# Kernel tuning notes

Measured on AMD Instinct MI355X. Metric: run time of the kernel, lower is better.

## Reference

```python
import jax, jax.numpy as jnp
import numpy as np

H, D = 16, 64  # num_heads, head_dim (d_model = 1024)


def setup_inputs() -> dict:
    key = jax.random.key(0)
    ks = jax.random.split(key, 5)
    B, S, E = 2, 2048, H * D
    scale = 0.02  # keep logits in a sane range
    return {
        "x": jax.random.normal(ks[0], (B, S, E), jnp.float32),
        "Wq": jax.random.normal(ks[1], (E, E), jnp.float32) * scale,
        "bq": jnp.zeros((E,), jnp.float32),
        "Wk": jax.random.normal(ks[2], (E, E), jnp.float32) * scale,
        "bk": jnp.zeros((E,), jnp.float32),
        "Wv": jax.random.normal(ks[3], (E, E), jnp.float32) * scale,
        "bv": jnp.zeros((E,), jnp.float32),
        "Wo": jax.random.normal(ks[4], (E, E), jnp.float32) * scale,
        "bo": jnp.zeros((E,), jnp.float32),
    }


def reference(x, Wq, bq, Wk, bk, Wv, bv, Wo, bo):
    B, S, E = x.shape

    def proj(W, b):
        # torch nn.Linear: x @ W.T + b; then split heads -> [B, H, S, D]
        return (x @ W.T + b).reshape(B, S, H, D).transpose(0, 2, 1, 3)

    q = proj(Wq, bq)
    k = proj(Wk, bk)
    v = proj(Wv, bv)

    # scores [B, H, S, S]; original masks with -inf BEFORE scaling (-inf/scale == -inf)
    att = jnp.einsum("bhqd,bhkd->bhqk", q, k)
    causal = jnp.triu(jnp.ones((S, S), bool), k=1)  # True above diagonal
    att = jnp.where(causal, -jnp.inf, att) * jnp.float32(1.0 / np.sqrt(D))
    att = jax.nn.softmax(att, axis=-1)

    ctx = jnp.einsum("bhqk,bhkd->bhqd", att, v)  # [B, H, S, D]
    ctx = ctx.transpose(0, 2, 1, 3).reshape(B, S, H * D)  # merge heads
    return ctx @ Wo.T + bo
```

## Files before the change

kernel.cpp:

```cpp
#include <hip/hip_runtime.h>
#include <hip/hip_bf16.h>

#define S_LEN 2048
#define NH    16
#define HD    64
#define EMB   1024
#define BATCH 2
#define M_TOT 4096

typedef __attribute__((ext_vector_type(8)))  __bf16   bf16x8;
typedef __attribute__((ext_vector_type(4)))  __bf16   bf16x4;
typedef __attribute__((ext_vector_type(4)))  float    f32x4;
typedef __attribute__((ext_vector_type(16))) float    f32x16;
typedef __attribute__((ext_vector_type(4)))  unsigned u32x4;

static __device__ __forceinline__ unsigned pk2(float a, float b) {
    unsigned short ua = __builtin_bit_cast(unsigned short, (__bf16)a);
    unsigned short ub = __builtin_bit_cast(unsigned short, (__bf16)b);
    return (unsigned)ua | ((unsigned)ub << 16);
}

__global__ __launch_bounds__(256) void cast_all(const float* __restrict__ x,
        const float* __restrict__ wq, const float* __restrict__ wk,
        const float* __restrict__ wv, const float* __restrict__ wo,
        __bf16* __restrict__ xb, __bf16* __restrict__ wqb,
        __bf16* __restrict__ wkb, __bf16* __restrict__ wvb,
        __bf16* __restrict__ wob) {
    int i = blockIdx.x * 256 + threadIdx.x;
    const float* src; __bf16* dst; int j;
    if (i < (1 << 20)) { src = x; dst = xb; j = i; }
    else {
        int t = i - (1 << 20);
        int r = t >> 18;
        j = t & ((1 << 18) - 1);
        src = (r == 0) ? wq : (r == 1) ? wk : (r == 2) ? wv : wo;
        dst = (r == 0) ? wqb : (r == 1) ? wkb : (r == 2) ? wvb : wob;
    }
    f32x4 v = ((const f32x4*)src)[j];
    bf16x4 o;
    o[0] = (__bf16)v[0]; o[1] = (__bf16)v[1];
    o[2] = (__bf16)v[2]; o[3] = (__bf16)v[3];
    ((bf16x4*)dst)[j] = o;
}

#define GEMM_STAGE(Abuf, Bbuf, Asrc, Bsrc, k0)                                            \
    _Pragma("unroll")                                                                     \
    for (int t = 0; t < 4; ++t) {                                                         \
        const int row = wid * 32 + t * 8;                                                 \
        __builtin_amdgcn_global_load_lds(                                                 \
            (const __attribute__((address_space(1))) void*)&Asrc[(size_t)(m0 + row + lr8) * EMB + (k0) + lc8], \
            (__attribute__((address_space(3))) void*)&Abuf[row][0], 16, 0, 0);            \
        __builtin_amdgcn_global_load_lds(                                                 \
            (const __attribute__((address_space(1))) void*)&Bsrc[(size_t)(n0 + row + lr8) * EMB + (k0) + lc8], \
            (__attribute__((address_space(3))) void*)&Bbuf[row][0], 16, 0, 0);            \
    }

#define GEMM_COMPUTE(Abuf, Bbuf)                                                          \
    _Pragma("unroll")                                                                     \
    for (int kk = 0; kk < 2; ++kk) {                                                      \
        bf16x8 af[4], bfr[4];                                                             \
        _Pragma("unroll")                                                                 \
        for (int i = 0; i < 4; ++i)                                                       \
            af[i] = *(const bf16x8*)&Abuf[wr * 64 + i * 16 + lrow][kk * 32 + lhi * 8];    \
        _Pragma("unroll")                                                                 \
        for (int j = 0; j < 4; ++j)                                                       \
            bfr[j] = *(const bf16x8*)&Bbuf[wc * 64 + j * 16 + lrow][kk * 32 + lhi * 8];   \
        _Pragma("unroll")                                                                 \
        for (int i = 0; i < 4; ++i)                                                       \
            _Pragma("unroll")                                                             \
            for (int j = 0; j < 4; ++j)                                                   \
                acc[i][j] = __builtin_amdgcn_mfma_f32_16x16x32_bf16(af[i], bfr[j], acc[i][j], 0, 0, 0); \
    }

__global__ __launch_bounds__(256) void gemm_qkv(const __bf16* __restrict__ A,
        const __bf16* __restrict__ Wq, const __bf16* __restrict__ Wk,
        const __bf16* __restrict__ Wv,
        const float* __restrict__ bq, const float* __restrict__ bk,
        const float* __restrict__ bv,
        __bf16* __restrict__ Qo, __bf16* __restrict__ Ko, __bf16* __restrict__ Vo) {
    __shared__ __bf16 As0[128][64], As1[128][64];
    __shared__ __bf16 Bs0[128][64], Bs1[128][64];

    const int z = blockIdx.z;
    const __bf16* Bw   = (z == 0) ? Wq : (z == 1) ? Wk : Wv;
    const float*  bias = (z == 0) ? bq : (z == 1) ? bk : bv;
    __bf16*       outp = (z == 0) ? Qo : (z == 1) ? Ko : Vo;

    const int tid  = threadIdx.x;
    const int wid  = tid >> 6;
    const int lane = tid & 63;
    const int lrow = lane & 15;
    const int lhi  = lane >> 4;
    const int m0 = blockIdx.y * 128;
    const int n0 = blockIdx.x * 128;
    const int wr = wid >> 1, wc = wid & 1;
    const int lr8 = lane >> 3;
    const int lc8 = (lane & 7) * 8;

    f32x4 acc[4][4];
#pragma unroll
    for (int i = 0; i < 4; ++i)
#pragma unroll
        for (int j = 0; j < 4; ++j)
            acc[i][j] = (f32x4){0.f, 0.f, 0.f, 0.f};

    GEMM_STAGE(As0, Bs0, A, Bw, 0)
    __syncthreads();
    for (int kt = 0; kt < 16; kt += 2) {
        GEMM_STAGE(As1, Bs1, A, Bw, (kt + 1) * 64)
        GEMM_COMPUTE(As0, Bs0)
        __syncthreads();
        if (kt + 2 < 16) { GEMM_STAGE(As0, Bs0, A, Bw, (kt + 2) * 64) }
        GEMM_COMPUTE(As1, Bs1)
        __syncthreads();
    }

#pragma unroll
    for (int i = 0; i < 4; ++i) {
#pragma unroll
        for (int j = 0; j < 4; ++j) {
#pragma unroll
            for (int jj = 0; jj < 4; ++jj) {
                int row = m0 + wr * 64 + i * 16 + lhi * 4 + jj;
                int col = n0 + wc * 64 + j * 16 + lrow;
                float v = acc[i][j][jj] + bias[col];
                int b = row >> 11, s = row & (S_LEN - 1);
                int h = col >> 6,  d = col & (HD - 1);
                size_t idx = (z == 2)
                    ? ((size_t)(b * NH + h) * HD + d) * S_LEN + s
                    : ((size_t)(b * NH + h) * S_LEN + s) * HD + d;
                outp[idx] = (__bf16)v;
            }
        }
    }
}

__global__ __launch_bounds__(256) void gemm_out(const __bf16* __restrict__ A,
        const __bf16* __restrict__ Bw, const float* __restrict__ bias,
        float* __restrict__ outp) {
    __shared__ __bf16 As0[128][64], As1[128][64];
    __shared__ __bf16 Bs0[128][64], Bs1[128][64];

    const int tid  = threadIdx.x;
    const int wid  = tid >> 6;
    const int lane = tid & 63;
    const int lrow = lane & 15;
    const int lhi  = lane >> 4;
    const int m0 = blockIdx.y * 128;
    const int n0 = blockIdx.x * 128;
    const int wr = wid >> 1, wc = wid & 1;
    const int lr8 = lane >> 3;
    const int lc8 = (lane & 7) * 8;

    f32x4 acc[4][4];
#pragma unroll
    for (int i = 0; i < 4; ++i)
#pragma unroll
        for (int j = 0; j < 4; ++j)
            acc[i][j] = (f32x4){0.f, 0.f, 0.f, 0.f};

    GEMM_STAGE(As0, Bs0, A, Bw, 0)
    __syncthreads();
    for (int kt = 0; kt < 16; kt += 2) {
        GEMM_STAGE(As1, Bs1, A, Bw, (kt + 1) * 64)
        GEMM_COMPUTE(As0, Bs0)
        __syncthreads();
        if (kt + 2 < 16) { GEMM_STAGE(As0, Bs0, A, Bw, (kt + 2) * 64) }
        GEMM_COMPUTE(As1, Bs1)
        __syncthreads();
    }

#pragma unroll
    for (int i = 0; i < 4; ++i)
#pragma unroll
        for (int j = 0; j < 4; ++j)
#pragma unroll
            for (int jj = 0; jj < 4; ++jj) {
                int row = m0 + wr * 64 + i * 16 + lhi * 4 + jj;
                int col = n0 + wc * 64 + j * 16 + lrow;
                outp[(size_t)row * EMB + col] = acc[i][j][jj] + bias[col];
            }
}

__global__ __launch_bounds__(256) void attn_kernel(const __bf16* __restrict__ Q,
        const __bf16* __restrict__ K, const __bf16* __restrict__ Vt,
        __bf16* __restrict__ ctx) {
    __shared__ float Of[4][32][65];
    __shared__ float MLs[4][2][32];

    const int wid  = threadIdx.x >> 6;
    const int lane = threadIdx.x & 63;
    const int lq   = lane & 31;
    const int hi   = lane >> 5;
    const int bid  = blockIdx.x;
    const int xcd  = bid & 7;
    const int idx  = bid >> 3;
    const int qt   = 63 - (idx & 63);
    const int bh   = xcd + 8 * (idx >> 6);
    const int q0   = qt * 32;

    const __bf16* Qh = Q  + (size_t)bh * S_LEN * HD;
    const __bf16* Kh = K  + (size_t)bh * S_LEN * HD;
    const __bf16* Vh = Vt + (size_t)bh * HD * S_LEN;

    bf16x8 qf[4];
#pragma unroll
    for (int ds = 0; ds < 4; ++ds) {
        bf16x8 t = *(const bf16x8*)&Qh[(size_t)(q0 + lq) * HD + ds * 16 + hi * 8];
#pragma unroll
        for (int j = 0; j < 8; ++j) qf[ds][j] = (__bf16)((float)t[j] * 0.125f);
    }

    f32x16 o0, o1;
#pragma unroll
    for (int r = 0; r < 16; ++r) { o0[r] = 0.f; o1[r] = 0.f; }
    float m = -1e30f, l = 0.f;

    const int nkt = qt + 1;

    bf16x8 kf0, kf1, kf2, kf3;
    if (wid < nkt) {
        const __bf16* kp = &Kh[(size_t)(wid * 32 + lq) * HD + hi * 8];
        kf0 = *(const bf16x8*)(kp);      kf1 = *(const bf16x8*)(kp + 16);
        kf2 = *(const bf16x8*)(kp + 32); kf3 = *(const bf16x8*)(kp + 48);
    }

    for (int kt = wid; kt < nkt; kt += 4) {
        const int kk0 = kt * 32;

        bf16x8 va0 = *(const bf16x8*)&Vh[(size_t)lq * S_LEN + kk0 + hi * 8];
        bf16x8 vb0 = *(const bf16x8*)&Vh[(size_t)lq * S_LEN + kk0 + 16 + hi * 8];
        bf16x8 va1 = *(const bf16x8*)&Vh[(size_t)(32 + lq) * S_LEN + kk0 + hi * 8];
        bf16x8 vb1 = *(const bf16x8*)&Vh[(size_t)(32 + lq) * S_LEN + kk0 + 16 + hi * 8];

        const int nk0 = (kt + 4 < nkt ? kt + 4 : kt) * 32;
        bf16x8 nkf0, nkf1, nkf2, nkf3;
        {
            const __bf16* kp = &Kh[(size_t)(nk0 + lq) * HD + hi * 8];
            nkf0 = *(const bf16x8*)(kp);      nkf1 = *(const bf16x8*)(kp + 16);
            nkf2 = *(const bf16x8*)(kp + 32); nkf3 = *(const bf16x8*)(kp + 48);
        }

        f32x16 s;
#pragma unroll
        for (int r = 0; r < 16; ++r) s[r] = 0.f;
        s = __builtin_amdgcn_mfma_f32_32x32x16_bf16(kf0, qf[0], s, 0, 0, 0);
        s = __builtin_amdgcn_mfma_f32_32x32x16_bf16(kf1, qf[1], s, 0, 0, 0);
        s = __builtin_amdgcn_mfma_f32_32x32x16_bf16(kf2, qf[2], s, 0, 0, 0);
        s = __builtin_amdgcn_mfma_f32_32x32x16_bf16(kf3, qf[3], s, 0, 0, 0);

        if (kk0 == q0) {
#pragma unroll
            for (int r = 0; r < 16; ++r) {
                int keyl = (r & 3) + 8 * (r >> 2) + 4 * hi;
                s[r] = (keyl <= lq) ? s[r] : -1e30f;
            }
        }

        float pm = s[0];
#pragma unroll
        for (int r = 1; r < 16; ++r) pm = fmaxf(pm, s[r]);
        pm = fmaxf(pm, __shfl_xor(pm, 32));

        if (!__all(pm - m <= 8.f)) {
            float mn = fmaxf(m, pm);
            float f  = __expf(m - mn);
            l *= f;
#pragma unroll
            for (int r = 0; r < 16; ++r) { o0[r] *= f; o1[r] *= f; }
            m = mn;
        }

        float ps = 0.f;
#pragma unroll
        for (int r = 0; r < 16; ++r) { s[r] = __expf(s[r] - m); ps += s[r]; }
        ps += __shfl_xor(ps, 32);
        l += ps;

        unsigned w0 = pk2(s[0],  s[1]),  w1 = pk2(s[2],  s[3]);
        unsigned w2 = pk2(s[4],  s[5]),  w3 = pk2(s[6],  s[7]);
        unsigned w4 = pk2(s[8],  s[9]),  w5 = pk2(s[10], s[11]);
        unsigned w6 = pk2(s[12], s[13]), w7 = pk2(s[14], s[15]);

        unsigned e0 = (unsigned)__shfl_xor((int)(hi ? w0 : w2), 32);
        unsigned e1 = (unsigned)__shfl_xor((int)(hi ? w1 : w3), 32);
        unsigned e2 = (unsigned)__shfl_xor((int)(hi ? w4 : w6), 32);
        unsigned e3 = (unsigned)__shfl_xor((int)(hi ? w5 : w7), 32);
        u32x4 pb0, pb1;
        pb0[0] = hi ? e0 : w0;  pb0[1] = hi ? e1 : w1;
        pb0[2] = hi ? w2 : e0;  pb0[3] = hi ? w3 : e1;
        pb1[0] = hi ? e2 : w4;  pb1[1] = hi ? e3 : w5;
        pb1[2] = hi ? w6 : e2;  pb1[3] = hi ? w7 : e3;
        bf16x8 pb0b = __builtin_bit_cast(bf16x8, pb0);
        bf16x8 pb1b = __builtin_bit_cast(bf16x8, pb1);

        o0 = __builtin_amdgcn_mfma_f32_32x32x16_bf16(va0, pb0b, o0, 0, 0, 0);
        o0 = __builtin_amdgcn_mfma_f32_32x32x16_bf16(vb0, pb1b, o0, 0, 0, 0);
        o1 = __builtin_amdgcn_mfma_f32_32x32x16_bf16(va1, pb0b, o1, 0, 0, 0);
        o1 = __builtin_amdgcn_mfma_f32_32x32x16_bf16(vb1, pb1b, o1, 0, 0, 0);

        kf0 = nkf0; kf1 = nkf1; kf2 = nkf2; kf3 = nkf3;
    }

#pragma unroll
    for (int r = 0; r < 16; ++r) {
        int d0 = (r & 3) + 8 * (r >> 2) + 4 * hi;
        Of[wid][lq][d0]      = o0[r];
        Of[wid][lq][32 + d0] = o1[r];
    }
    if (lane < 32) { MLs[wid][0][lq] = m; MLs[wid][1][lq] = l; }
    __syncthreads();

    {
        const int tq = threadIdx.x >> 3;
        const int d8 = (threadIdx.x & 7) * 8;
        float m0_ = MLs[0][0][tq], m1_ = MLs[1][0][tq];
        float m2_ = MLs[2][0][tq], m3_ = MLs[3][0][tq];
        float M = fmaxf(fmaxf(m0_, m1_), fmaxf(m2_, m3_));
        float a0 = __expf(m0_ - M), a1 = __expf(m1_ - M);
        float a2 = __expf(m2_ - M), a3 = __expf(m3_ - M);
        float L = MLs[0][1][tq] * a0 + MLs[1][1][tq] * a1
                + MLs[2][1][tq] * a2 + MLs[3][1][tq] * a3;
        float invL = 1.f / L;
        const int b = bh >> 4, h = bh & 15;
        bf16x8 outv;
#pragma unroll
        for (int e = 0; e < 8; ++e) {
            int d = d8 + e;
            float v = a0 * Of[0][tq][d] + a1 * Of[1][tq][d]
                    + a2 * Of[2][tq][d] + a3 * Of[3][tq][d];
            outv[e] = (__bf16)(v * invL);
        }
        *(bf16x8*)&ctx[((size_t)b * S_LEN + q0 + tq) * EMB + h * HD + d8] = outv;
    }
}

extern "C" void kernel_launch(void* const* d_in, const int* in_sizes, int n_in,
                              void* d_out, int out_size, void* d_ws, size_t ws_size,
                              hipStream_t stream) {
    const float* x  = (const float*)d_in[0];
    const float* Wq = (const float*)d_in[1];
    const float* bq = (const float*)d_in[2];
    const float* Wk = (const float*)d_in[3];
    const float* bk = (const float*)d_in[4];
    const float* Wv = (const float*)d_in[5];
    const float* bv = (const float*)d_in[6];
    const float* Wo = (const float*)d_in[7];
    const float* bo = (const float*)d_in[8];

    char* ws = (char*)d_ws;
    __bf16* xb  = (__bf16*)(ws);
    __bf16* Wqb = (__bf16*)(ws + ( 8ull << 20));
    __bf16* Wkb = (__bf16*)(ws + (10ull << 20));
    __bf16* Wvb = (__bf16*)(ws + (12ull << 20));
    __bf16* Wob = (__bf16*)(ws + (14ull << 20));
    __bf16* Qb  = (__bf16*)(ws + (16ull << 20));
    __bf16* Kb  = (__bf16*)(ws + (24ull << 20));
    __bf16* Vtb = (__bf16*)(ws + (32ull << 20));
    __bf16* Cb  = (__bf16*)(ws + (40ull << 20));

    cast_all<<<8192, 256, 0, stream>>>(x, Wq, Wk, Wv, Wo, xb, Wqb, Wkb, Wvb, Wob);

    gemm_qkv<<<dim3(EMB / 128, M_TOT / 128, 3), 256, 0, stream>>>(
        xb, Wqb, Wkb, Wvb, bq, bk, bv, Qb, Kb, Vtb);

    attn_kernel<<<dim3(2048), 256, 0, stream>>>(Qb, Kb, Vtb, Cb);

    gemm_out<<<dim3(EMB / 128, M_TOT / 128), 256, 0, stream>>>(Cb, Wob, bo, (float*)d_out);
}
```

Measured before the change: 238.8 us.

## Fuse Q/K/V projections into one GEMM kernel sharing the A tile

Replaces the three-way z-dimension launch of the QKV GEMM with a single 512-thread block that loads one activation tile and three weight tiles, computing Q, K and V accumulators together. This cuts redundant loads of the activation matrix across the three projections. In exchange it drops the previous LDS double-buffering, so global-to-LDS loads are no longer overlapped with MFMA compute. The grid also shrinks to a third as many blocks, and each block holds more accumulator registers.

Result: faster. 232.6 us (-2.6%).

```diff
diff --git a/kernel.cpp b/kernel.cpp
--- a/kernel.cpp
+++ b/kernel.cpp
@@ -43,6 +43,115 @@
     ((bf16x4*)dst)[j] = o;
 }
 
+__global__ __launch_bounds__(512) void gemm_qkv(const __bf16* __restrict__ A,
+        const __bf16* __restrict__ Wq, const __bf16* __restrict__ Wk,
+        const __bf16* __restrict__ Wv,
+        const float* __restrict__ bq, const float* __restrict__ bk,
+        const float* __restrict__ bv,
+        __bf16* __restrict__ Qo, __bf16* __restrict__ Ko, __bf16* __restrict__ Vo) {
+    __shared__ __bf16 As [128][64];
+    __shared__ __bf16 Bqs[128][64];
+    __shared__ __bf16 Bks[128][64];
+    __shared__ __bf16 Bvs[128][64];
+
+    const int tid  = threadIdx.x;
+    const int wid  = tid >> 6;
+    const int lane = tid & 63;
+    const int lrow = lane & 15;
+    const int lhi  = lane >> 4;
+    const int m0 = blockIdx.y * 128;
+    const int n0 = blockIdx.x * 128;
+    const int wr = wid >> 2, wc = wid & 3;
+    const int lr8 = lane >> 3;
+    const int lc8 = (lane & 7) * 8;
+
+    f32x4 aq[4][2], ak[4][2], av[4][2];
+#pragma unroll
+    for (int i = 0; i < 4; ++i)
+#pragma unroll
+        for (int j = 0; j < 2; ++j) {
+            aq[i][j] = (f32x4){0.f, 0.f, 0.f, 0.f};
+            ak[i][j] = (f32x4){0.f, 0.f, 0.f, 0.f};
+            av[i][j] = (f32x4){0.f, 0.f, 0.f, 0.f};
+        }
+
+    for (int kt = 0; kt < 16; ++kt) {
+        const int k0 = kt * 64;
+#pragma unroll
+        for (int t = 0; t < 2; ++t) {
+            const int row = wid * 16 + t * 8;
+            __builtin_amdgcn_global_load_lds(
+                (const __attribute__((address_space(1))) void*)&A [(size_t)(m0 + row + lr8) * EMB + k0 + lc8],
+                (__attribute__((address_space(3))) void*)&As[row][0], 16, 0, 0);
+            __builtin_amdgcn_global_load_lds(
+                (const __attribute__((address_space(1))) void*)&Wq[(size_t)(n0 + row + lr8) * EMB + k0 + lc8],
+                (__attribute__((address_space(3))) void*)&Bqs[row][0], 16, 0, 0);
+            __builtin_amdgcn_global_load_lds(
+                (const __attribute__((address_space(1))) void*)&Wk[(size_t)(n0 + row + lr8) * EMB + k0 + lc8],
+                (__attribute__((address_space(3))) void*)&Bks[row][0], 16, 0, 0);
+            __builtin_amdgcn_global_load_lds(
+                (const __attribute__((address_space(1))) void*)&Wv[(size_t)(n0 + row + lr8) * EMB + k0 + lc8],
+                (__attribute__((address_space(3))) void*)&Bvs[row][0], 16, 0, 0);
+        }
+        __syncthreads();
+#pragma unroll
+        for (int kk = 0; kk < 2; ++kk) {
+            bf16x8 af[4];
+#pragma unroll
+            for (int i = 0; i < 4; ++i)
+                af[i] = *(const bf16x8*)&As[wr * 64 + i * 16 + lrow][kk * 32 + lhi * 8];
+            bf16x8 bfr[2];
+#pragma unroll
+            for (int j = 0; j < 2; ++j)
+                bfr[j] = *(const bf16x8*)&Bqs[wc * 32 + j * 16 + lrow][kk * 32 + lhi * 8];
+#pragma unroll
+            for (int i = 0; i < 4; ++i)
+#pragma unroll
+                for (int j = 0; j < 2; ++j)
+                    aq[i][j] = __builtin_amdgcn_mfma_f32_16x16x32_bf16(af[i], bfr[j], aq[i][j], 0, 0, 0);
+#pragma unroll
+            for (int j = 0; j < 2; ++j)
+                bfr[j] = *(const bf16x8*)&Bks[wc * 32 + j * 16 + lrow][kk * 32 + lhi * 8];
+#pragma unroll
+            for (int i = 0; i < 4; ++i)
+#pragma unroll
+                for (int j = 0; j < 2; ++j)
+                    ak[i][j] = __builtin_amdgcn_mfma_f32_16x16x32_bf16(af[i], bfr[j], ak[i][j], 0, 0, 0);
+#pragma unroll
+            for (int j = 0; j < 2; ++j)
+                bfr[j] = *(const bf16x8*)&Bvs[wc * 32 + j * 16 + lrow][kk * 32 + lhi * 8];
+#pragma unroll
+            for (int i = 0; i < 4; ++i)
+#pragma unroll
+                for (int j = 0; j < 2; ++j)
+                    av[i][j] = __builtin_amdgcn_mfma_f32_16x16x32_bf16(af[i], bfr[j], av[i][j], 0, 0, 0);
+        }
+        __syncthreads();
+    }
+
+#define QKV_EPI(ACC, OUTP, BIASP, ISV)                                            \
+    _Pragma("unroll")                                                             \
+    for (int i = 0; i < 4; ++i)                                                   \
+        _Pragma("unroll")                                                         \
+        for (int j = 0; j < 2; ++j)                                               \
+            _Pragma("unroll")                                                     \
+            for (int jj = 0; jj < 4; ++jj) {                                      \
+                int row = m0 + wr * 64 + i * 16 + lhi * 4 + jj;                   \
+                int col = n0 + wc * 32 + j * 16 + lrow;                           \
+                float v = ACC[i][j][jj] + BIASP[col];                             \
+                int b = row >> 11, s = row & (S_LEN - 1);                         \
+                int h = col >> 6,  d = col & (HD - 1);                            \
+                size_t idx = (ISV)                                                \
+                    ? ((size_t)(b * NH + h) * HD + d) * S_LEN + s                 \
+                    : ((size_t)(b * NH + h) * S_LEN + s) * HD + d;                \
+                OUTP[idx] = (__bf16)v;                                            \
+            }
+    QKV_EPI(aq, Qo, bq, 0)
+    QKV_EPI(ak, Ko, bk, 0)
+    QKV_EPI(av, Vo, bv, 1)
+#undef QKV_EPI
+}
+
 #define GEMM_STAGE(Abuf, Bbuf, Asrc, Bsrc, k0)                                            \
     _Pragma("unroll")                                                                     \
     for (int t = 0; t < 4; ++t) {                                                         \
@@ -72,69 +181,6 @@
                 acc[i][j] = __builtin_amdgcn_mfma_f32_16x16x32_bf16(af[i], bfr[j], acc[i][j], 0, 0, 0); \
     }
 
-__global__ __launch_bounds__(256) void gemm_qkv(const __bf16* __restrict__ A,
-        const __bf16* __restrict__ Wq, const __bf16* __restrict__ Wk,
-        const __bf16* __restrict__ Wv,
-        const float* __restrict__ bq, const float* __restrict__ bk,
-        const float* __restrict__ bv,
-        __bf16* __restrict__ Qo, __bf16* __restrict__ Ko, __bf16* __restrict__ Vo) {
-    __shared__ __bf16 As0[128][64], As1[128][64];
-    __shared__ __bf16 Bs0[128][64], Bs1[128][64];
-
-    const int z = blockIdx.z;
-    const __bf16* Bw   = (z == 0) ? Wq : (z == 1) ? Wk : Wv;
-    const float*  bias = (z == 0) ? bq : (z == 1) ? bk : bv;
-    __bf16*       outp = (z == 0) ? Qo : (z == 1) ? Ko : Vo;
-
-    const int tid  = threadIdx.x;
-    const int wid  = tid >> 6;
-    const int lane = tid & 63;
-    const int lrow = lane & 15;
-    const int lhi  = lane >> 4;
-    const int m0 = blockIdx.y * 128;
-    const int n0 = blockIdx.x * 128;
-    const int wr = wid >> 1, wc = wid & 1;
-    const int lr8 = lane >> 3;
-    const int lc8 = (lane & 7) * 8;
-
-    f32x4 acc[4][4];
-#pragma unroll
-    for (int i = 0; i < 4; ++i)
-#pragma unroll
-        for (int j = 0; j < 4; ++j)
-            acc[i][j] = (f32x4){0.f, 0.f, 0.f, 0.f};
-
-    GEMM_STAGE(As0, Bs0, A, Bw, 0)
-    __syncthreads();
-    for (int kt = 0; kt < 16; kt += 2) {
-        GEMM_STAGE(As1, Bs1, A, Bw, (kt + 1) * 64)
-        GEMM_COMPUTE(As0, Bs0)
-        __syncthreads();
-        if (kt + 2 < 16) { GEMM_STAGE(As0, Bs0, A, Bw, (kt + 2) * 64) }
-        GEMM_COMPUTE(As1, Bs1)
-        __syncthreads();
-    }
-
-#pragma unroll
-    for (int i = 0; i < 4; ++i) {
-#pragma unroll
-        for (int j = 0; j < 4; ++j) {
-#pragma unroll
-            for (int jj = 0; jj < 4; ++jj) {
-                int row = m0 + wr * 64 + i * 16 + lhi * 4 + jj;
-                int col = n0 + wc * 64 + j * 16 + lrow;
-                float v = acc[i][j][jj] + bias[col];
-                int b = row >> 11, s = row & (S_LEN - 1);
-                int h = col >> 6,  d = col & (HD - 1);
-                size_t idx = (z == 2)
-                    ? ((size_t)(b * NH + h) * HD + d) * S_LEN + s
-                    : ((size_t)(b * NH + h) * S_LEN + s) * HD + d;
-                outp[idx] = (__bf16)v;
-            }
-        }
-    }
-}
-
 __global__ __launch_bounds__(256) void gemm_out(const __bf16* __restrict__ A,
         const __bf16* __restrict__ Bw, const float* __restrict__ bias,
         float* __restrict__ outp) {
@@ -361,7 +407,7 @@
 
     cast_all<<<8192, 256, 0, stream>>>(x, Wq, Wk, Wv, Wo, xb, Wqb, Wkb, Wvb, Wob);
 
-    gemm_qkv<<<dim3(EMB / 128, M_TOT / 128, 3), 256, 0, stream>>>(
+    gemm_qkv<<<dim3(EMB / 128, M_TOT / 128), 512, 0, stream>>>(
         xb, Wqb, Wkb, Wvb, bq, bk, bv, Qb, Kb, Vtb);
 
     attn_kernel<<<dim3(2048), 256, 0, stream>>>(Qb, Kb, Vtb, Cb);
```
